# Optimization experiments

Hardware: AMD Instinct MI355X
Metric: run time of the kernel (lower is better)

Reference implementation:

```python
import jax, jax.numpy as jnp
import numpy as np

BS, GRID, LSTM_H, CNN_C, PROJ = 256, 49, 512, 2048, 512


def setup_inputs() -> dict:
    key = jax.random.key(0)
    ks = jax.random.split(key, 7)
    s = lambda fan_in: 1.0 / np.sqrt(fan_in)
    return {
        "lstm_hidden": jax.random.normal(ks[0], (BS, LSTM_H), jnp.float32),
        "cnn_feat": jax.random.normal(ks[1], (BS, GRID, CNN_C), jnp.float32),
        "W_lstm": jax.random.normal(ks[2], (PROJ, LSTM_H), jnp.float32) * s(LSTM_H),
        "b_lstm": jax.random.normal(ks[3], (PROJ,), jnp.float32) * s(LSTM_H),
        "W_cnn": jax.random.normal(ks[4], (PROJ, CNN_C), jnp.float32) * s(CNN_C),
        "b_cnn": jax.random.normal(ks[5], (PROJ,), jnp.float32) * s(CNN_C),
        "w_attn": jax.random.normal(ks[6], (1, PROJ), jnp.float32) * s(PROJ),
    }


def reference(lstm_hidden, cnn_feat, W_lstm, b_lstm, W_cnn, b_cnn, w_attn):
    # H computed once (original loop recomputes it per grid, identically)
    H = lstm_hidden @ W_lstm.T + b_lstm                       # (bs, P)
    V = jnp.einsum("bgc,pc->bgp", cnn_feat, W_cnn) + b_cnn    # (bs, G, P)
    z = jnp.tanh(H[:, None, :] + V) @ w_attn[0]               # (bs, G)
    bs, G = z.shape
    # Faithful to torch: cat over grids along dim 0 -> (G*bs,), then view(bs, G)
    z_scrambled = jnp.swapaxes(z, 0, 1).reshape(bs, G)
    return jax.nn.softmax(z_scrambled, axis=1)
```

## Files before the change

kernel.cpp:

```cpp
#include <hip/hip_runtime.h>
#include <math.h>

#define BSZ    256
#define GRID_N 49
#define LSTMH  512
#define CNN_C  2048
#define PROJ   512
#define KAUG   2560
#define M_TOT  12544
#define BK     64
#define KTILES (KAUG / BK)

#define MT2    128
#define NT2    128
#define NBLK2  ((M_TOT / MT2) * (PROJ / NT2))

#define MT     64
#define NT     128
#define NBLK   ((M_TOT / MT) * (PROJ / NT))

#define ACHUNKS (M_TOT * CNN_C / 8)
#define LCHUNKS (BSZ * LSTMH / 8)
#define ABLK    ((ACHUNKS + LCHUNKS) / 256)
#define WBLK    640
#define PBLK    (ABLK + WBLK)

typedef short bf16x8 __attribute__((ext_vector_type(8)));
typedef float f32x4  __attribute__((ext_vector_type(4)));

static __device__ __forceinline__ unsigned short bf16_rne(float f) {
    unsigned int u = __float_as_uint(f);
    u = u + 0x7FFFu + ((u >> 16) & 1u);
    return (unsigned short)(u >> 16);
}
static __device__ __forceinline__ uint4 pack8f(const float* f) {
    uint4 o;
    o.x = (unsigned int)bf16_rne(f[0]) | ((unsigned int)bf16_rne(f[1]) << 16);
    o.y = (unsigned int)bf16_rne(f[2]) | ((unsigned int)bf16_rne(f[3]) << 16);
    o.z = (unsigned int)bf16_rne(f[4]) | ((unsigned int)bf16_rne(f[5]) << 16);
    o.w = (unsigned int)bf16_rne(f[6]) | ((unsigned int)bf16_rne(f[7]) << 16);
    return o;
}
static __device__ __forceinline__ float tanh_fast(float x) {
    float e = __expf(2.f * x);
    return 1.f - 2.f / (e + 1.f);
}
static __device__ __forceinline__ void glds16(const void* g, void* l) {
    __builtin_amdgcn_global_load_lds(
        (const __attribute__((address_space(1))) unsigned int*)g,
        (__attribute__((address_space(3))) unsigned int*)l, 16, 0, 0);
}

__global__ __launch_bounds__(256) void prep_all(
    const float* __restrict__ cnn, const float* __restrict__ lstm,
    const float* __restrict__ Wc,  const float* __restrict__ Wl,
    unsigned short* __restrict__ wsW, unsigned short* __restrict__ wsA,
    unsigned short* __restrict__ wsL, float* __restrict__ out)
{
    const int bid = blockIdx.x, t = threadIdx.x;
    if (bid < 49) out[bid * 256 + t] = 0.f;
    float f[8];
    if (bid < ABLK) {
        const int c = bid * 256 + t;
        const float* src; unsigned short* dst;
        if (c < ACHUNKS) { src = cnn  + (size_t)c * 8; dst = wsA + (size_t)c * 8; }
        else { const int c2 = c - ACHUNKS; src = lstm + (size_t)c2 * 8; dst = wsL + (size_t)c2 * 8; }
        *(float4*)&f[0] = ((const float4*)src)[0];
        *(float4*)&f[4] = ((const float4*)src)[1];
        *(uint4*)dst = pack8f(f);
    } else {
        const int c  = (bid - ABLK) * 256 + t;
        const int p  = c / 320;
        const int kc = (c % 320) * 8;
        const float* src = (kc < CNN_C) ? (Wc + (size_t)p * CNN_C + kc)
                                        : (Wl + (size_t)p * LSTMH + (kc - CNN_C));
        *(float4*)&f[0] = ((const float4*)src)[0];
        *(float4*)&f[4] = ((const float4*)src)[1];
        *(uint4*)(wsW + (size_t)p * KAUG + kc) = pack8f(f);
    }
}

__global__ __launch_bounds__(256, 4) void gemm5(
    const unsigned short* __restrict__ wsW, const unsigned short* __restrict__ wsA,
    const unsigned short* __restrict__ wsL,
    const float* __restrict__ bl, const float* __restrict__ bc,
    const float* __restrict__ wat, float* __restrict__ out)
{
    __shared__ unsigned short Ash[MT2][BK];
    __shared__ unsigned short Bsh[NT2][BK];

    const int t   = threadIdx.x;
    const int w   = t >> 6;
    const int l   = t & 63;
    const int q   = l >> 4;
    const int r16 = l & 15;
    const int wr  = w >> 1;
    const int wc  = w & 1;

    const int bid = (int)blockIdx.x;
    const int swz = (bid & 7) * (NBLK2 / 8) + (bid >> 3);
    const int m0  = (swz >> 2) * MT2;
    const int n0  = (swz & 3) * NT2;

    const int srow = l >> 3;
    const int cg   = (l & 7) ^ srow;

    auto stage = [&](int kt) {
        const int k0 = kt * BK;
        #pragma unroll
        for (int j = 0; j < 4; ++j) {
            const int rowb = w * 32 + j * 8;
            const unsigned short* g = wsW + (size_t)(n0 + rowb + srow) * KAUG + k0 + cg * 8;
            glds16(g, &Bsh[rowb][0]);
        }
        if (k0 < CNN_C) {
            #pragma unroll
            for (int j = 0; j < 4; ++j) {
                const int rowa = w * 32 + j * 8;
                const unsigned short* g = wsA + (size_t)(m0 + rowa + srow) * CNN_C + k0 + cg * 8;
                glds16(g, &Ash[rowa][0]);
            }
        } else {
            const int k0l = k0 - CNN_C;
            #pragma unroll
            for (int j = 0; j < 4; ++j) {
                const int rowa = w * 32 + j * 8;
                const int rg   = m0 + rowa + srow;
                const unsigned short* g = wsL + (size_t)(rg / 49) * LSTMH + k0l + cg * 8;
                glds16(g, &Ash[rowa][0]);
            }
        }
    };

    f32x4 acc[4][4];
    #pragma unroll
    for (int mt = 0; mt < 4; ++mt)
        #pragma unroll
        for (int nt = 0; nt < 4; ++nt)
            acc[mt][nt] = (f32x4){0.f, 0.f, 0.f, 0.f};

    stage(0);

    for (int kt = 0; kt < KTILES; ++kt) {
        asm volatile("s_waitcnt vmcnt(0)" ::: "memory");
        __builtin_amdgcn_s_barrier();
        #pragma unroll
        for (int ks = 0; ks < 2; ++ks) {
            const int cp = ((ks * 4 + q) ^ (r16 & 7)) * 8;
            bf16x8 af[4], bfr[4];
            #pragma unroll
            for (int mt = 0; mt < 4; ++mt)
                af[mt] = *(const bf16x8*)&Ash[wr * 64 + mt * 16 + r16][cp];
            #pragma unroll
            for (int nt = 0; nt < 4; ++nt)
                bfr[nt] = *(const bf16x8*)&Bsh[wc * 64 + nt * 16 + r16][cp];
            #pragma unroll
            for (int mt = 0; mt < 4; ++mt)
                #pragma unroll
                for (int nt = 0; nt < 4; ++nt)
                    acc[mt][nt] = __builtin_amdgcn_mfma_f32_16x16x32_bf16(
                        af[mt], bfr[nt], acc[mt][nt], 0, 0, 0);
        }
        __builtin_amdgcn_s_barrier();
        if (kt + 1 < KTILES) stage(kt + 1);
    }

    float* zpf = (float*)&Ash[0][0];
    float part[4][4];
    #pragma unroll
    for (int mt = 0; mt < 4; ++mt)
        #pragma unroll
        for (int rr = 0; rr < 4; ++rr) part[mt][rr] = 0.f;
    #pragma unroll
    for (int nt = 0; nt < 4; ++nt) {
        const int p = n0 + wc * 64 + nt * 16 + r16;
        const float bb = bl[p] + bc[p];
        const float wa = wat[p];
        #pragma unroll
        for (int mt = 0; mt < 4; ++mt)
            #pragma unroll
            for (int rr = 0; rr < 4; ++rr)
                part[mt][rr] += tanh_fast(acc[mt][nt][rr] + bb) * wa;
    }
    #pragma unroll
    for (int mt = 0; mt < 4; ++mt)
        #pragma unroll
        for (int rr = 0; rr < 4; ++rr) {
            float v = part[mt][rr];
            v += __shfl_xor(v, 1);
            v += __shfl_xor(v, 2);
            v += __shfl_xor(v, 4);
            v += __shfl_xor(v, 8);
            if (r16 == 0) zpf[wc * MT2 + wr * 64 + mt * 16 + q * 4 + rr] = v;
        }
    __syncthreads();
    if (t < MT2) {
        const float v = zpf[t] + zpf[MT2 + t];
        const int row = m0 + t;
        const int b2  = row / 49;
        const int g2  = row - b2 * 49;
        atomicAdd(&out[g2 * BSZ + b2], v);
    }
}

__global__ __launch_bounds__(256, 4) void gemm_k(
    const float* __restrict__ lstm, const float* __restrict__ cnn,
    const float* __restrict__ Wc,   const float* __restrict__ Wl,
    const float* __restrict__ bl,   const float* __restrict__ bc,
    const float* __restrict__ wat,  float* __restrict__ out)
{
    __shared__ unsigned short Ash[MT][BK];
    __shared__ unsigned short Bsh[NT][BK];
    __shared__ float zp[4][MT];

    const int t   = threadIdx.x;
    const int w   = t >> 6;
    const int l   = t & 63;
    const int q   = l >> 4;
    const int r16 = l & 15;

    const int bid = (int)blockIdx.x;
    const int swz = (bid & 7) * (NBLK / 8) + (bid >> 3);
    const int m0 = (swz >> 2) * MT;
    const int n0 = (swz & 3) * NT;

    const int ra  = t >> 2;
    const int ca0 = t & 3;
    const int sa  = ra & 7;
    const int grow = m0 + ra;
    const int ab   = grow / 49;
    const int ag   = grow - ab * 49;
    const float* cnnb  = cnn + ((size_t)ab * GRID_N + ag) * CNN_C;
    const float* lstmb = lstm + (size_t)ab * LSTMH;

    f32x4 acc[4][2];
    #pragma unroll
    for (int mt = 0; mt < 4; ++mt)
        #pragma unroll
        for (int nt = 0; nt < 2; ++nt)
            acc[mt][nt] = (f32x4){0.f, 0.f, 0.f, 0.f};

    float4 fa0, fa1, fa2, fa3;

    auto a_load = [&](int k0) {
        const float* s = (k0 < CNN_C) ? (cnnb + k0) : (lstmb + (k0 - CNN_C));
        const float4* p0 = (const float4*)(s + ca0 * 8);
        const float4* p1 = (const float4*)(s + (ca0 + 4) * 8);
        fa0 = p0[0]; fa1 = p0[1];
        fa2 = p1[0]; fa3 = p1[1];
    };
    auto a_write = [&]() {
        float f[8];
        *(float4*)&f[0] = fa0; *(float4*)&f[4] = fa1;
        *(uint4*)&Ash[ra][(ca0 ^ sa) * 8] = pack8f(f);
        *(float4*)&f[0] = fa2; *(float4*)&f[4] = fa3;
        *(uint4*)&Ash[ra][((ca0 + 4) ^ sa) * 8] = pack8f(f);
    };
    auto b_stage = [&](int k0) {
        const int rb = t >> 1;
        const int hb = t & 1;
        const float* s = (k0 < CNN_C) ? (Wc + (size_t)(n0 + rb) * CNN_C + k0)
                                      : (Wl + (size_t)(n0 + rb) * LSTMH + (k0 - CNN_C));
        const int sw = rb & 7;
        #pragma unroll
        for (int c = 0; c < 4; ++c) {
            const int cc = hb * 4 + c;
            float f[8];
            *(float4*)&f[0] = ((const float4*)(s + cc * 8))[0];
            *(float4*)&f[4] = ((const float4*)(s + cc * 8))[1];
            *(uint4*)&Bsh[rb][(cc ^ sw) * 8] = pack8f(f);
        }
    };

    a_load(0);
    a_write();
    b_stage(0);

    for (int kt = 0; kt < KTILES; ++kt) {
        __syncthreads();
        const bool more = (kt + 1 < KTILES);
        if (more) a_load((kt + 1) * BK);
        #pragma unroll
        for (int ks = 0; ks < 2; ++ks) {
            const int cp = ((ks * 4 + q) ^ (r16 & 7)) * 8;
            bf16x8 af[4], bfr[2];
            #pragma unroll
            for (int mt = 0; mt < 4; ++mt)
                af[mt] = *(const bf16x8*)&Ash[mt * 16 + r16][cp];
            #pragma unroll
            for (int nt = 0; nt < 2; ++nt)
                bfr[nt] = *(const bf16x8*)&Bsh[w * 32 + nt * 16 + r16][cp];
            #pragma unroll
            for (int mt = 0; mt < 4; ++mt)
                #pragma unroll
                for (int nt = 0; nt < 2; ++nt)
                    acc[mt][nt] = __builtin_amdgcn_mfma_f32_16x16x32_bf16(
                        af[mt], bfr[nt], acc[mt][nt], 0, 0, 0);
        }
        __syncthreads();
        if (more) { a_write(); b_stage((kt + 1) * BK); }
    }

    float part[4][4];
    #pragma unroll
    for (int mt = 0; mt < 4; ++mt)
        #pragma unroll
        for (int rr = 0; rr < 4; ++rr) part[mt][rr] = 0.f;
    #pragma unroll
    for (int nt = 0; nt < 2; ++nt) {
        const int p = n0 + w * 32 + nt * 16 + r16;
        const float bb = bl[p] + bc[p];
        const float wa = wat[p];
        #pragma unroll
        for (int mt = 0; mt < 4; ++mt)
            #pragma unroll
            for (int rr = 0; rr < 4; ++rr)
                part[mt][rr] += tanh_fast(acc[mt][nt][rr] + bb) * wa;
    }
    #pragma unroll
    for (int mt = 0; mt < 4; ++mt)
        #pragma unroll
        for (int rr = 0; rr < 4; ++rr) {
            float v = part[mt][rr];
            v += __shfl_xor(v, 1);
            v += __shfl_xor(v, 2);
            v += __shfl_xor(v, 4);
            v += __shfl_xor(v, 8);
            if (r16 == 0) zp[w][mt * 16 + q * 4 + rr] = v;
        }
    __syncthreads();
    if (t < MT) {
        const float v = zp[0][t] + zp[1][t] + zp[2][t] + zp[3][t];
        const int row = m0 + t;
        const int b2  = row / 49;
        const int g2  = row - b2 * 49;
        atomicAdd(&out[g2 * BSZ + b2], v);
    }
}

__global__ __launch_bounds__(64) void softmax_rows(float* __restrict__ out)
{
    const int i = blockIdx.x;
    const int j = threadIdx.x;
    float x = (j < GRID_N) ? out[i * GRID_N + j] : -1e30f;
    float m = x;
    #pragma unroll
    for (int off = 32; off > 0; off >>= 1) m = fmaxf(m, __shfl_xor(m, off));
    float e = (j < GRID_N) ? __expf(x - m) : 0.f;
    float s = e;
    #pragma unroll
    for (int off = 32; off > 0; off >>= 1) s += __shfl_xor(s, off);
    if (j < GRID_N) out[i * GRID_N + j] = e / s;
}

extern "C" void kernel_launch(void* const* d_in, const int* in_sizes, int n_in,
                              void* d_out, int out_size, void* d_ws, size_t ws_size,
                              hipStream_t stream)
{
    const float* lstm = (const float*)d_in[0];
    const float* cnn  = (const float*)d_in[1];
    const float* Wl   = (const float*)d_in[2];
    const float* bl   = (const float*)d_in[3];
    const float* Wc   = (const float*)d_in[4];
    const float* bc   = (const float*)d_in[5];
    const float* wat  = (const float*)d_in[6];
    float* out = (float*)d_out;

    const size_t szW = (size_t)PROJ * KAUG * sizeof(unsigned short);
    const size_t szA = (size_t)M_TOT * CNN_C * sizeof(unsigned short);
    const size_t szL = (size_t)BSZ * LSTMH * sizeof(unsigned short);

    if (ws_size >= szW + szA + szL) {
        unsigned short* wsW = (unsigned short*)d_ws;
        unsigned short* wsA = wsW + (size_t)PROJ * KAUG;
        unsigned short* wsL = wsA + (size_t)M_TOT * CNN_C;
        prep_all<<<dim3(PBLK), dim3(256), 0, stream>>>(cnn, lstm, Wc, Wl, wsW, wsA, wsL, out);
        gemm5<<<dim3(NBLK2), dim3(256), 0, stream>>>(wsW, wsA, wsL, bl, bc, wat, out);
    } else {
        hipMemsetAsync(out, 0, (size_t)out_size * sizeof(float), stream);
        gemm_k<<<dim3(NBLK), dim3(256), 0, stream>>>(lstm, cnn, Wc, Wl, bl, bc, wat, out);
    }
    softmax_rows<<<dim3(BSZ), dim3(64), 0, stream>>>(out);
}
```

Measured before the change: 217.8 us.

## Double-buffer GEMM LDS tiles with two-deep prefetch and grid-stride prep kernel

The GEMM now keeps two LDS buffers for the A and B tiles and issues loads two k-tiles ahead. It waits with vmcnt(8) so the current tile's global-to-LDS copies finish while the next tile's stay in flight. This is meant to hide global load latency that the single-buffer wait-for-all loop exposed. Doubled LDS lowers occupancy (launch bounds 4 to 2). The prep conversion kernel becomes a fixed 2048-block grid-stride loop handling 16 elements per thread for the activations.

New measurement: 223.3 us. 1.03x slower.

```diff
diff --git a/kernel.cpp b/kernel.cpp
--- a/kernel.cpp
+++ b/kernel.cpp
@@ -19,11 +19,10 @@
 #define NT     128
 #define NBLK   ((M_TOT / MT) * (PROJ / NT))
 
-#define ACHUNKS (M_TOT * CNN_C / 8)
-#define LCHUNKS (BSZ * LSTMH / 8)
-#define ABLK    ((ACHUNKS + LCHUNKS) / 256)
-#define WBLK    640
-#define PBLK    (ABLK + WBLK)
+#define ACH16   (M_TOT * CNN_C / 16)
+#define LCH16   (BSZ * LSTMH / 16)
+#define WCH8    (PROJ * KAUG / 8)
+#define PGRID   2048
 
 typedef short bf16x8 __attribute__((ext_vector_type(8)));
 typedef float f32x4  __attribute__((ext_vector_type(4)));
@@ -51,43 +50,56 @@
         (__attribute__((address_space(3))) unsigned int*)l, 16, 0, 0);
 }
 
-__global__ __launch_bounds__(256) void prep_all(
+__global__ __launch_bounds__(256) void prep_all3(
     const float* __restrict__ cnn, const float* __restrict__ lstm,
     const float* __restrict__ Wc,  const float* __restrict__ Wl,
     unsigned short* __restrict__ wsW, unsigned short* __restrict__ wsA,
     unsigned short* __restrict__ wsL, float* __restrict__ out)
 {
     const int bid = blockIdx.x, t = threadIdx.x;
+    const int g0  = bid * 256 + t;
+    const int gs  = PGRID * 256;
     if (bid < 49) out[bid * 256 + t] = 0.f;
     float f[8];
-    if (bid < ABLK) {
-        const int c = bid * 256 + t;
-        const float* src; unsigned short* dst;
-        if (c < ACHUNKS) { src = cnn  + (size_t)c * 8; dst = wsA + (size_t)c * 8; }
-        else { const int c2 = c - ACHUNKS; src = lstm + (size_t)c2 * 8; dst = wsL + (size_t)c2 * 8; }
-        *(float4*)&f[0] = ((const float4*)src)[0];
-        *(float4*)&f[4] = ((const float4*)src)[1];
-        *(uint4*)dst = pack8f(f);
-    } else {
-        const int c  = (bid - ABLK) * 256 + t;
+    for (int c = g0; c < ACH16; c += gs) {
+        const float* s = cnn + (size_t)c * 16;
+        unsigned short* d = wsA + (size_t)c * 16;
+        *(float4*)&f[0] = ((const float4*)s)[0];
+        *(float4*)&f[4] = ((const float4*)s)[1];
+        *(uint4*)d = pack8f(f);
+        *(float4*)&f[0] = ((const float4*)s)[2];
+        *(float4*)&f[4] = ((const float4*)s)[3];
+        *(uint4*)(d + 8) = pack8f(f);
+    }
+    for (int c = g0; c < LCH16; c += gs) {
+        const float* s = lstm + (size_t)c * 16;
+        unsigned short* d = wsL + (size_t)c * 16;
+        *(float4*)&f[0] = ((const float4*)s)[0];
+        *(float4*)&f[4] = ((const float4*)s)[1];
+        *(uint4*)d = pack8f(f);
+        *(float4*)&f[0] = ((const float4*)s)[2];
+        *(float4*)&f[4] = ((const float4*)s)[3];
+        *(uint4*)(d + 8) = pack8f(f);
+    }
+    for (int c = g0; c < WCH8; c += gs) {
         const int p  = c / 320;
         const int kc = (c % 320) * 8;
-        const float* src = (kc < CNN_C) ? (Wc + (size_t)p * CNN_C + kc)
-                                        : (Wl + (size_t)p * LSTMH + (kc - CNN_C));
-        *(float4*)&f[0] = ((const float4*)src)[0];
-        *(float4*)&f[4] = ((const float4*)src)[1];
+        const float* s = (kc < CNN_C) ? (Wc + (size_t)p * CNN_C + kc)
+                                      : (Wl + (size_t)p * LSTMH + (kc - CNN_C));
+        *(float4*)&f[0] = ((const float4*)s)[0];
+        *(float4*)&f[4] = ((const float4*)s)[1];
         *(uint4*)(wsW + (size_t)p * KAUG + kc) = pack8f(f);
     }
 }
 
-__global__ __launch_bounds__(256, 4) void gemm5(
+__global__ __launch_bounds__(256, 2) void gemm8(
     const unsigned short* __restrict__ wsW, const unsigned short* __restrict__ wsA,
     const unsigned short* __restrict__ wsL,
     const float* __restrict__ bl, const float* __restrict__ bc,
     const float* __restrict__ wat, float* __restrict__ out)
 {
-    __shared__ unsigned short Ash[MT2][BK];
-    __shared__ unsigned short Bsh[NT2][BK];
+    __shared__ unsigned short Ab[2][MT2][BK];
+    __shared__ unsigned short Bb[2][NT2][BK];
 
     const int t   = threadIdx.x;
     const int w   = t >> 6;
@@ -105,20 +117,20 @@
     const int srow = l >> 3;
     const int cg   = (l & 7) ^ srow;
 
-    auto stage = [&](int kt) {
+    auto stage = [&](int kt, int bufi) {
         const int k0 = kt * BK;
         #pragma unroll
         for (int j = 0; j < 4; ++j) {
             const int rowb = w * 32 + j * 8;
             const unsigned short* g = wsW + (size_t)(n0 + rowb + srow) * KAUG + k0 + cg * 8;
-            glds16(g, &Bsh[rowb][0]);
+            glds16(g, &Bb[bufi][rowb][0]);
         }
         if (k0 < CNN_C) {
             #pragma unroll
             for (int j = 0; j < 4; ++j) {
                 const int rowa = w * 32 + j * 8;
                 const unsigned short* g = wsA + (size_t)(m0 + rowa + srow) * CNN_C + k0 + cg * 8;
-                glds16(g, &Ash[rowa][0]);
+                glds16(g, &Ab[bufi][rowa][0]);
             }
         } else {
             const int k0l = k0 - CNN_C;
@@ -127,7 +139,7 @@
                 const int rowa = w * 32 + j * 8;
                 const int rg   = m0 + rowa + srow;
                 const unsigned short* g = wsL + (size_t)(rg / 49) * LSTMH + k0l + cg * 8;
-                glds16(g, &Ash[rowa][0]);
+                glds16(g, &Ab[bufi][rowa][0]);
             }
         }
     };
@@ -139,10 +151,16 @@
         for (int nt = 0; nt < 4; ++nt)
             acc[mt][nt] = (f32x4){0.f, 0.f, 0.f, 0.f};
 
-    stage(0);
+    stage(0, 0);
+    stage(1, 1);
 
     for (int kt = 0; kt < KTILES; ++kt) {
-        asm volatile("s_waitcnt vmcnt(0)" ::: "memory");
+        const int cur = kt & 1;
+        if (kt + 1 < KTILES) {
+            asm volatile("s_waitcnt vmcnt(8)" ::: "memory");
+        } else {
+            asm volatile("s_waitcnt vmcnt(0)" ::: "memory");
+        }
         __builtin_amdgcn_s_barrier();
         #pragma unroll
         for (int ks = 0; ks < 2; ++ks) {
@@ -150,10 +168,10 @@
             bf16x8 af[4], bfr[4];
             #pragma unroll
             for (int mt = 0; mt < 4; ++mt)
-                af[mt] = *(const bf16x8*)&Ash[wr * 64 + mt * 16 + r16][cp];
+                af[mt] = *(const bf16x8*)&Ab[cur][wr * 64 + mt * 16 + r16][cp];
             #pragma unroll
             for (int nt = 0; nt < 4; ++nt)
-                bfr[nt] = *(const bf16x8*)&Bsh[wc * 64 + nt * 16 + r16][cp];
+                bfr[nt] = *(const bf16x8*)&Bb[cur][wc * 64 + nt * 16 + r16][cp];
             #pragma unroll
             for (int mt = 0; mt < 4; ++mt)
                 #pragma unroll
@@ -162,10 +180,10 @@
                         af[mt], bfr[nt], acc[mt][nt], 0, 0, 0);
         }
         __builtin_amdgcn_s_barrier();
-        if (kt + 1 < KTILES) stage(kt + 1);
-    }
-
-    float* zpf = (float*)&Ash[0][0];
+        if (kt + 2 < KTILES) stage(kt + 2, cur);
+    }
+
+    float* zpf = (float*)&Ab[0][0][0];
     float part[4][4];
     #pragma unroll
     for (int mt = 0; mt < 4; ++mt)
@@ -374,8 +392,8 @@
         unsigned short* wsW = (unsigned short*)d_ws;
         unsigned short* wsA = wsW + (size_t)PROJ * KAUG;
         unsigned short* wsL = wsA + (size_t)M_TOT * CNN_C;
-        prep_all<<<dim3(PBLK), dim3(256), 0, stream>>>(cnn, lstm, Wc, Wl, wsW, wsA, wsL, out);
-        gemm5<<<dim3(NBLK2), dim3(256), 0, stream>>>(wsW, wsA, wsL, bl, bc, wat, out);
+        prep_all3<<<dim3(PGRID), dim3(256), 0, stream>>>(cnn, lstm, Wc, Wl, wsW, wsA, wsL, out);
+        gemm8<<<dim3(NBLK2), dim3(256), 0, stream>>>(wsW, wsA, wsL, bl, bc, wat, out);
     } else {
         hipMemsetAsync(out, 0, (size_t)out_size * sizeof(float), stream);
         gemm_k<<<dim3(NBLK), dim3(256), 0, stream>>>(lstm, cnn, Wc, Wl, bl, bc, wat, out);
```

## Double-buffer LDS tiles in bf16 GEMM to overlap global loads with MFMA

Applied to the files above, without the earlier changes.

Splits the A and B shared-memory tiles into two buffers and prefetches two K-tiles ahead. The loop then waits with a partial vmcnt so the next tile's direct-to-LDS loads stay in flight while MFMAs run on the current buffer. This targets the load latency exposed by the old single-buffer wait-all-then-compute loop. LDS use doubles and launch bounds drop from 4 to 2 blocks per CU, which may reduce occupancy.

After: 212.3 us. 2.5% less time.

```diff
diff --git a/kernel.cpp b/kernel.cpp
--- a/kernel.cpp
+++ b/kernel.cpp
@@ -80,14 +80,14 @@
     }
 }
 
-__global__ __launch_bounds__(256, 4) void gemm5(
+__global__ __launch_bounds__(256, 2) void gemm8(
     const unsigned short* __restrict__ wsW, const unsigned short* __restrict__ wsA,
     const unsigned short* __restrict__ wsL,
     const float* __restrict__ bl, const float* __restrict__ bc,
     const float* __restrict__ wat, float* __restrict__ out)
 {
-    __shared__ unsigned short Ash[MT2][BK];
-    __shared__ unsigned short Bsh[NT2][BK];
+    __shared__ unsigned short Ab[2][MT2][BK];
+    __shared__ unsigned short Bb[2][NT2][BK];
 
     const int t   = threadIdx.x;
     const int w   = t >> 6;
@@ -105,20 +105,20 @@
     const int srow = l >> 3;
     const int cg   = (l & 7) ^ srow;
 
-    auto stage = [&](int kt) {
+    auto stage = [&](int kt, int bufi) {
         const int k0 = kt * BK;
         #pragma unroll
         for (int j = 0; j < 4; ++j) {
             const int rowb = w * 32 + j * 8;
             const unsigned short* g = wsW + (size_t)(n0 + rowb + srow) * KAUG + k0 + cg * 8;
-            glds16(g, &Bsh[rowb][0]);
+            glds16(g, &Bb[bufi][rowb][0]);
         }
         if (k0 < CNN_C) {
             #pragma unroll
             for (int j = 0; j < 4; ++j) {
                 const int rowa = w * 32 + j * 8;
                 const unsigned short* g = wsA + (size_t)(m0 + rowa + srow) * CNN_C + k0 + cg * 8;
-                glds16(g, &Ash[rowa][0]);
+                glds16(g, &Ab[bufi][rowa][0]);
             }
         } else {
             const int k0l = k0 - CNN_C;
@@ -127,7 +127,7 @@
                 const int rowa = w * 32 + j * 8;
                 const int rg   = m0 + rowa + srow;
                 const unsigned short* g = wsL + (size_t)(rg / 49) * LSTMH + k0l + cg * 8;
-                glds16(g, &Ash[rowa][0]);
+                glds16(g, &Ab[bufi][rowa][0]);
             }
         }
     };
@@ -139,10 +139,16 @@
         for (int nt = 0; nt < 4; ++nt)
             acc[mt][nt] = (f32x4){0.f, 0.f, 0.f, 0.f};
 
-    stage(0);
+    stage(0, 0);
+    stage(1, 1);
 
     for (int kt = 0; kt < KTILES; ++kt) {
-        asm volatile("s_waitcnt vmcnt(0)" ::: "memory");
+        const int cur = kt & 1;
+        if (kt + 1 < KTILES) {
+            asm volatile("s_waitcnt vmcnt(8)" ::: "memory");
+        } else {
+            asm volatile("s_waitcnt vmcnt(0)" ::: "memory");
+        }
         __builtin_amdgcn_s_barrier();
         #pragma unroll
         for (int ks = 0; ks < 2; ++ks) {
@@ -150,10 +156,10 @@
             bf16x8 af[4], bfr[4];
             #pragma unroll
             for (int mt = 0; mt < 4; ++mt)
-                af[mt] = *(const bf16x8*)&Ash[wr * 64 + mt * 16 + r16][cp];
+                af[mt] = *(const bf16x8*)&Ab[cur][wr * 64 + mt * 16 + r16][cp];
             #pragma unroll
             for (int nt = 0; nt < 4; ++nt)
-                bfr[nt] = *(const bf16x8*)&Bsh[wc * 64 + nt * 16 + r16][cp];
+                bfr[nt] = *(const bf16x8*)&Bb[cur][wc * 64 + nt * 16 + r16][cp];
             #pragma unroll
             for (int mt = 0; mt < 4; ++mt)
                 #pragma unroll
@@ -162,10 +168,10 @@
                         af[mt], bfr[nt], acc[mt][nt], 0, 0, 0);
         }
         __builtin_amdgcn_s_barrier();
-        if (kt + 1 < KTILES) stage(kt + 1);
-    }
-
-    float* zpf = (float*)&Ash[0][0];
+        if (kt + 2 < KTILES) stage(kt + 2, cur);
+    }
+
+    float* zpf = (float*)&Ab[0][0][0];
     float part[4][4];
     #pragma unroll
     for (int mt = 0; mt < 4; ++mt)
@@ -375,7 +381,7 @@
         unsigned short* wsA = wsW + (size_t)PROJ * KAUG;
         unsigned short* wsL = wsA + (size_t)M_TOT * CNN_C;
         prep_all<<<dim3(PBLK), dim3(256), 0, stream>>>(cnn, lstm, Wc, Wl, wsW, wsA, wsL, out);
-        gemm5<<<dim3(NBLK2), dim3(256), 0, stream>>>(wsW, wsA, wsL, bl, bc, wat, out);
+        gemm8<<<dim3(NBLK2), dim3(256), 0, stream>>>(wsW, wsA, wsL, bl, bc, wat, out);
     } else {
         hipMemsetAsync(out, 0, (size_t)out_size * sizeof(float), stream);
         gemm_k<<<dim3(NBLK), dim3(256), 0, stream>>>(lstm, cnn, Wc, Wl, bl, bc, wat, out);
```
